# Kernel tuning notes

Measured on AMD Instinct MI355X. Metric: run time of the kernel, lower is better.

The kernel has to match this reference:

```python
import jax, jax.numpy as jnp
import numpy as np

# Fano plane lines (i, j, k): colonies whose octonion product should close, e_i * e_j ~ e_k
FANO = np.array([[0, 1, 3], [1, 2, 4], [2, 3, 5], [3, 4, 6], [4, 5, 0], [5, 6, 1], [6, 0, 2]], dtype=np.int64)


def _oct_structure():
    """8x8x8 structure constants M with (x*y)_k = sum_ij M[i,j,k] x_i y_j,
    built via Cayley-Dickson doubling of quaternions (true octonion multiply)."""
    def qmul(a, b):
        w1, x1, y1, z1 = a
        w2, x2, y2, z2 = b
        return np.array([
            w1 * w2 - x1 * x2 - y1 * y2 - z1 * z2,
            w1 * x2 + x1 * w2 + y1 * z2 - z1 * y2,
            w1 * y2 - x1 * z2 + y1 * w2 + z1 * x2,
            w1 * z2 + x1 * y2 - y1 * x2 + z1 * w2,
        ])

    def qconj(a):
        return a * np.array([1.0, -1.0, -1.0, -1.0])

    M = np.zeros((8, 8, 8), dtype=np.float32)
    I = np.eye(8, dtype=np.float32)
    for i in range(8):
        for j in range(8):
            a1, a2 = I[i, :4], I[i, 4:]
            b1, b2 = I[j, :4], I[j, 4:]
            c1 = qmul(a1, b1) - qmul(qconj(b2), a2)
            c2 = qmul(b2, a1) + qmul(a2, qconj(b1))
            M[i, j] = np.concatenate([c1, c2])
    return M


_M_NP = _oct_structure()


def setup_inputs() -> dict:
    key = jax.random.key(0)
    k1, = jax.random.split(key, 1)
    B = 1048576
    colony_states = jax.random.normal(k1, (B, 7, 8), dtype=jnp.float32)
    log_sensitivity = jnp.ones((), dtype=jnp.float32)  # nn.Parameter init 1.0
    return {"colony_states": colony_states, "log_sensitivity": log_sensitivity}


def reference(colony_states, log_sensitivity):
    M = jnp.asarray(_M_NP, dtype=colony_states.dtype)  # [8,8,8]
    # F.normalize(p=2, dim=-1): x / max(||x||, 1e-12)
    norm = jnp.maximum(jnp.linalg.norm(colony_states, axis=-1, keepdims=True), 1e-12)
    states = colony_states / norm  # [B,7,8]

    xi = states[:, FANO[:, 0]]  # [B,7,8]
    xj = states[:, FANO[:, 1]]  # [B,7,8]
    xk = states[:, FANO[:, 2]]  # [B,7,8]

    # All 7 Fano-line octonion products in one bilinear contraction
    prod = jnp.einsum('bli,blj,ijk->blk', xi, xj, M)  # [B,7,8]
    total_error = jnp.sum((prod - xk) ** 2, axis=(-1, -2))  # [B]
    avg_error = total_error / 7.0
    phi = -jnp.log(avg_error + 1e-8) * jnp.exp(log_sensitivity)
    return jnp.clip(phi, 0.0, 10.0)
```

## Files before the change

kernel.cpp:

```cpp
#include <hip/hip_runtime.h>
#include <math.h>

__device__ __forceinline__ void qmul(float w1, float x1, float y1, float z1,
                                     float w2, float x2, float y2, float z2,
                                     float& w, float& x, float& y, float& z) {
    w = w1 * w2 - x1 * x2 - y1 * y2 - z1 * z2;
    x = w1 * x2 + x1 * w2 + y1 * z2 - z1 * y2;
    y = w1 * y2 - x1 * z2 + y1 * w2 + z1 * x2;
    z = w1 * z2 + x1 * y2 - y1 * x2 + z1 * w2;
}

__global__ __launch_bounds__(256) void oct_fano_kernel(
    const float* __restrict__ in,
    const float* __restrict__ logs,
    float* __restrict__ out,
    int B) {
    int b = blockIdx.x * 256 + threadIdx.x;
    if (b >= B) return;

    float x[7][8];
    const float4* p = (const float4*)(in + (size_t)b * 56);
#pragma unroll
    for (int k = 0; k < 14; k++) {
        float4 v = p[k];
        int r = k >> 1;
        int c = (k & 1) * 4;
        x[r][c + 0] = v.x;
        x[r][c + 1] = v.y;
        x[r][c + 2] = v.z;
        x[r][c + 3] = v.w;
    }

#pragma unroll
    for (int r = 0; r < 7; r++) {
        float s = 0.f;
#pragma unroll
        for (int c = 0; c < 8; c++) s += x[r][c] * x[r][c];
        float n = fmaxf(sqrtf(s), 1e-12f);
        float inv = 1.0f / n;
#pragma unroll
        for (int c = 0; c < 8; c++) x[r][c] *= inv;
    }

    float total = 0.f;
#pragma unroll
    for (int l = 0; l < 7; l++) {
        const float* a = x[l];
        const float* bb = x[(l + 1) % 7];
        const float* ck = x[(l + 3) % 7];

        float p0, p1, p2, p3, p4, p5, p6, p7;
        float t0, t1, t2, t3;
        qmul(a[0], a[1], a[2], a[3], bb[0], bb[1], bb[2], bb[3], p0, p1, p2, p3);
        qmul(bb[4], -bb[5], -bb[6], -bb[7], a[4], a[5], a[6], a[7], t0, t1, t2, t3);
        p0 -= t0; p1 -= t1; p2 -= t2; p3 -= t3;
        qmul(bb[4], bb[5], bb[6], bb[7], a[0], a[1], a[2], a[3], p4, p5, p6, p7);
        qmul(a[4], a[5], a[6], a[7], bb[0], -bb[1], -bb[2], -bb[3], t0, t1, t2, t3);
        p4 += t0; p5 += t1; p6 += t2; p7 += t3;

        float d0 = p0 - ck[0], d1 = p1 - ck[1], d2 = p2 - ck[2], d3 = p3 - ck[3];
        float d4 = p4 - ck[4], d5 = p5 - ck[5], d6 = p6 - ck[6], d7 = p7 - ck[7];
        total += d0 * d0 + d1 * d1 + d2 * d2 + d3 * d3 +
                 d4 * d4 + d5 * d5 + d6 * d6 + d7 * d7;
    }

    float avg = total * (1.0f / 7.0f);
    float phi = -logf(avg + 1e-8f) * expf(logs[0]);
    phi = fminf(fmaxf(phi, 0.0f), 10.0f);
    out[b] = phi;
}

extern "C" void kernel_launch(void* const* d_in, const int* in_sizes, int n_in,
                              void* d_out, int out_size, void* d_ws, size_t ws_size,
                              hipStream_t stream) {
    const float* states = (const float*)d_in[0];
    const float* logs = (const float*)d_in[1];
    float* out = (float*)d_out;
    int B = in_sizes[0] / 56;
    int blocks = (B + 255) / 256;
    oct_fano_kernel<<<blocks, 256, 0, stream>>>(states, logs, out, B);
}
```

Before: 312.8 us.

## Stage input through LDS with coalesced direct global-to-LDS loads

Before, each thread read its own 224-byte item with strided float4 loads, so the loads within a wavefront were poorly coalesced. Now each 64-thread block loads 64 items contiguously into shared memory using global_load_lds: each instruction moves 1 KB across lanes. Each thread then reads its item from LDS. Block size drops to 64 threads, and the 14 KB of LDS per block may limit occupancy. There is one barrier per block, and a slow fallback path handles the tail.

```diff
diff --git a/kernel.cpp b/kernel.cpp
--- a/kernel.cpp
+++ b/kernel.cpp
@@ -10,64 +10,92 @@
     z = w1 * z2 + x1 * y2 - y1 * x2 + z1 * w2;
 }
 
-__global__ __launch_bounds__(256) void oct_fano_kernel(
+#define ITEMS_PER_BLOCK 64
+#define F4_PER_ITEM 14
+#define BYTES_PER_ITEM 224
+
+__global__ __launch_bounds__(64) void oct_fano_kernel(
     const float* __restrict__ in,
     const float* __restrict__ logs,
     float* __restrict__ out,
     int B) {
-    int b = blockIdx.x * 256 + threadIdx.x;
-    if (b >= B) return;
+    __shared__ float4 tile[ITEMS_PER_BLOCK * F4_PER_ITEM];
 
-    float x[7][8];
-    const float4* p = (const float4*)(in + (size_t)b * 56);
+    const int lane = threadIdx.x;
+    const size_t base_item = (size_t)blockIdx.x * ITEMS_PER_BLOCK;
+    const char* gsrc = (const char*)in + base_item * BYTES_PER_ITEM;
+
+    if (base_item + ITEMS_PER_BLOCK <= (size_t)B) {
 #pragma unroll
-    for (int k = 0; k < 14; k++) {
-        float4 v = p[k];
-        int r = k >> 1;
-        int c = (k & 1) * 4;
-        x[r][c + 0] = v.x;
-        x[r][c + 1] = v.y;
-        x[r][c + 2] = v.z;
-        x[r][c + 3] = v.w;
+        for (int c = 0; c < F4_PER_ITEM; c++) {
+            __builtin_amdgcn_global_load_lds(
+                (const __attribute__((address_space(1))) void*)(gsrc + (size_t)c * 1024 + (size_t)lane * 16),
+                (__attribute__((address_space(3))) void*)((char*)tile + c * 1024),
+                16, 0, 0);
+        }
+    } else {
+        int items = B - (int)base_item;
+        if (items < 0) items = 0;
+        const float4* g4 = (const float4*)gsrc;
+        for (int idx = lane; idx < items * F4_PER_ITEM; idx += 64)
+            tile[idx] = g4[idx];
     }
+    asm volatile("s_waitcnt vmcnt(0)" ::: "memory");
+    __syncthreads();
+
+    const int b = (int)base_item + lane;
+    if (b < B) {
+        float x[7][8];
+        const float4* my = tile + lane * F4_PER_ITEM;
+#pragma unroll
+        for (int k = 0; k < F4_PER_ITEM; k++) {
+            float4 v = my[k];
+            int r = k >> 1;
+            int c = (k & 1) * 4;
+            x[r][c + 0] = v.x;
+            x[r][c + 1] = v.y;
+            x[r][c + 2] = v.z;
+            x[r][c + 3] = v.w;
+        }
 
 #pragma unroll
-    for (int r = 0; r < 7; r++) {
-        float s = 0.f;
+        for (int r = 0; r < 7; r++) {
+            float s = 0.f;
 #pragma unroll
-        for (int c = 0; c < 8; c++) s += x[r][c] * x[r][c];
-        float n = fmaxf(sqrtf(s), 1e-12f);
-        float inv = 1.0f / n;
+            for (int c = 0; c < 8; c++) s += x[r][c] * x[r][c];
+            float n = fmaxf(sqrtf(s), 1e-12f);
+            float inv = 1.0f / n;
 #pragma unroll
-        for (int c = 0; c < 8; c++) x[r][c] *= inv;
+            for (int c = 0; c < 8; c++) x[r][c] *= inv;
+        }
+
+        float total = 0.f;
+#pragma unroll
+        for (int l = 0; l < 7; l++) {
+            const float* a = x[l];
+            const float* bb = x[(l + 1) % 7];
+            const float* ck = x[(l + 3) % 7];
+
+            float p0, p1, p2, p3, p4, p5, p6, p7;
+            float t0, t1, t2, t3;
+            qmul(a[0], a[1], a[2], a[3], bb[0], bb[1], bb[2], bb[3], p0, p1, p2, p3);
+            qmul(bb[4], -bb[5], -bb[6], -bb[7], a[4], a[5], a[6], a[7], t0, t1, t2, t3);
+            p0 -= t0; p1 -= t1; p2 -= t2; p3 -= t3;
+            qmul(bb[4], bb[5], bb[6], bb[7], a[0], a[1], a[2], a[3], p4, p5, p6, p7);
+            qmul(a[4], a[5], a[6], a[7], bb[0], -bb[1], -bb[2], -bb[3], t0, t1, t2, t3);
+            p4 += t0; p5 += t1; p6 += t2; p7 += t3;
+
+            float d0 = p0 - ck[0], d1 = p1 - ck[1], d2 = p2 - ck[2], d3 = p3 - ck[3];
+            float d4 = p4 - ck[4], d5 = p5 - ck[5], d6 = p6 - ck[6], d7 = p7 - ck[7];
+            total += d0 * d0 + d1 * d1 + d2 * d2 + d3 * d3 +
+                     d4 * d4 + d5 * d5 + d6 * d6 + d7 * d7;
+        }
+
+        float avg = total * (1.0f / 7.0f);
+        float phi = -logf(avg + 1e-8f) * expf(logs[0]);
+        phi = fminf(fmaxf(phi, 0.0f), 10.0f);
+        out[b] = phi;
     }
-
-    float total = 0.f;
-#pragma unroll
-    for (int l = 0; l < 7; l++) {
-        const float* a = x[l];
-        const float* bb = x[(l + 1) % 7];
-        const float* ck = x[(l + 3) % 7];
-
-        float p0, p1, p2, p3, p4, p5, p6, p7;
-        float t0, t1, t2, t3;
-        qmul(a[0], a[1], a[2], a[3], bb[0], bb[1], bb[2], bb[3], p0, p1, p2, p3);
-        qmul(bb[4], -bb[5], -bb[6], -bb[7], a[4], a[5], a[6], a[7], t0, t1, t2, t3);
-        p0 -= t0; p1 -= t1; p2 -= t2; p3 -= t3;
-        qmul(bb[4], bb[5], bb[6], bb[7], a[0], a[1], a[2], a[3], p4, p5, p6, p7);
-        qmul(a[4], a[5], a[6], a[7], bb[0], -bb[1], -bb[2], -bb[3], t0, t1, t2, t3);
-        p4 += t0; p5 += t1; p6 += t2; p7 += t3;
-
-        float d0 = p0 - ck[0], d1 = p1 - ck[1], d2 = p2 - ck[2], d3 = p3 - ck[3];
-        float d4 = p4 - ck[4], d5 = p5 - ck[5], d6 = p6 - ck[6], d7 = p7 - ck[7];
-        total += d0 * d0 + d1 * d1 + d2 * d2 + d3 * d3 +
-                 d4 * d4 + d5 * d5 + d6 * d6 + d7 * d7;
-    }
-
-    float avg = total * (1.0f / 7.0f);
-    float phi = -logf(avg + 1e-8f) * expf(logs[0]);
-    phi = fminf(fmaxf(phi, 0.0f), 10.0f);
-    out[b] = phi;
 }
 
 extern "C" void kernel_launch(void* const* d_in, const int* in_sizes, int n_in,
@@ -77,6 +105,6 @@
     const float* logs = (const float*)d_in[1];
     float* out = (float*)d_out;
     int B = in_sizes[0] / 56;
-    int blocks = (B + 255) / 256;
-    oct_fano_kernel<<<blocks, 256, 0, stream>>>(states, logs, out, B);
+    int blocks = (B + ITEMS_PER_BLOCK - 1) / ITEMS_PER_BLOCK;
+    oct_fano_kernel<<<blocks, 64, 0, stream>>>(states, logs, out, B);
 }
```

Result: no change. 313.9 us (+0.4%).
